# Kernel optimization log

Measured on AMD Instinct MI355X. Metric: run time of the kernel, lower is better.

## Reference

```python
import jax, jax.numpy as jnp
import numpy as np

N, E = 20000, 100000
IN_CH, HID_CH, EDGE_DIM, NUM_CLASSES = 32, 32, 16, 10


def setup_inputs() -> dict:
    key = jax.random.key(0)
    ks = jax.random.split(key, 20)
    s = 0.05
    inp = {
        "x": jax.random.normal(ks[0], (N, IN_CH), jnp.float32),
        "edge_index": jax.random.randint(ks[1], (2, E), 0, N, jnp.int64),
        "edge_attr": jax.random.normal(ks[2], (E, EDGE_DIM), jnp.float32),
        # edge MLP 1: edge_dim -> in*hid -> in*hid (weights stored as (in, out))
        "e1_w1": jax.random.normal(ks[3], (EDGE_DIM, IN_CH * HID_CH), jnp.float32) * s,
        "e1_b1": jnp.zeros((IN_CH * HID_CH,), jnp.float32),
        "e1_w2": jax.random.normal(ks[4], (IN_CH * HID_CH, IN_CH * HID_CH), jnp.float32) * s,
        "e1_b2": jnp.zeros((IN_CH * HID_CH,), jnp.float32),
        "root1": jax.random.normal(ks[5], (IN_CH, HID_CH), jnp.float32) * s,
        "bias1": jnp.zeros((HID_CH,), jnp.float32),
        # edge MLP 2: edge_dim -> hid*hid -> hid*hid
        "e2_w1": jax.random.normal(ks[6], (EDGE_DIM, HID_CH * HID_CH), jnp.float32) * s,
        "e2_b1": jnp.zeros((HID_CH * HID_CH,), jnp.float32),
        "e2_w2": jax.random.normal(ks[7], (HID_CH * HID_CH, HID_CH * HID_CH), jnp.float32) * s,
        "e2_b2": jnp.zeros((HID_CH * HID_CH,), jnp.float32),
        "root2": jax.random.normal(ks[8], (HID_CH, HID_CH), jnp.float32) * s,
        "bias2": jnp.zeros((HID_CH,), jnp.float32),
        "lin_w": jax.random.normal(ks[9], (HID_CH, NUM_CLASSES), jnp.float32) * s,
        "lin_b": jnp.zeros((NUM_CLASSES,), jnp.float32),
    }
    return inp


def _nnconv_mean(x, src, dst, edge_attr, w1, b1, w2, b2, root, bias, in_ch, out_ch, n_nodes):
    # edge MLP -> per-edge weight matrix [E, in_ch, out_ch]
    h = jax.nn.relu(edge_attr @ w1 + b1) @ w2 + b2
    W = h.reshape(-1, in_ch, out_ch)
    # message: x_j @ W_e (gather source features, per-edge matmul)
    msg = jnp.einsum('ei,eio->eo', x[src], W)
    # scatter-mean to target nodes
    agg = jax.ops.segment_sum(msg, dst, num_segments=n_nodes)
    cnt = jax.ops.segment_sum(jnp.ones((msg.shape[0],), msg.dtype), dst, num_segments=n_nodes)
    mean = agg / jnp.maximum(cnt, 1.0)[:, None]
    return mean + x @ root + bias


def reference(x, edge_index, edge_attr,
              e1_w1, e1_b1, e1_w2, e1_b2, root1, bias1,
              e2_w1, e2_b1, e2_w2, e2_b2, root2, bias2,
              lin_w, lin_b):
    src, dst = edge_index[0], edge_index[1]
    n = x.shape[0]
    h = jax.nn.relu(_nnconv_mean(x, src, dst, edge_attr, e1_w1, e1_b1, e1_w2, e1_b2,
                                 root1, bias1, IN_CH, HID_CH, n))
    # dropout p=0.5 is identity in eval mode
    h = jax.nn.relu(_nnconv_mean(h, src, dst, edge_attr, e2_w1, e2_b1, e2_w2, e2_b2,
                                 root2, bias2, HID_CH, HID_CH, n))
    return h @ lin_w + lin_b
```

## Files before the change

kernel.cpp:

```cpp
#include <hip/hip_runtime.h>

typedef __attribute__((ext_vector_type(8))) short sh8;
typedef __attribute__((ext_vector_type(4))) float f32x4;

#define E_EDGES 100000
#define E_PAD   100096
#define N_NODES 20000

__device__ __forceinline__ unsigned short f2bf(float f) {
  union { float f; unsigned int u; } v; v.f = f;
  unsigned int r = v.u + 0x7FFFu + ((v.u >> 16) & 1u);
  return (unsigned short)(r >> 16);
}

__device__ __forceinline__ void async16(const void* g, void* l) {
  __builtin_amdgcn_global_load_lds((const __attribute__((address_space(1))) unsigned int*)g,
                                   (__attribute__((address_space(3))) unsigned int*)l,
                                   16, 0, 0);
}

__global__ void transpose_w2_kernel(const float* __restrict__ w2, unsigned short* __restrict__ w2t) {
  __shared__ float tile[32][33];
  int b = blockIdx.x;
  int bx = b & 31, by = b >> 5;
  int lx = threadIdx.x & 31, ly = threadIdx.x >> 5;
#pragma unroll
  for (int j = 0; j < 4; ++j)
    tile[ly + j*8][lx] = w2[(by*32 + ly + j*8)*1024 + bx*32 + lx];
  __syncthreads();
#pragma unroll
  for (int j = 0; j < 4; ++j)
    w2t[(size_t)(bx*32 + ly + j*8)*1024 + by*32 + lx] = f2bf(tile[lx][ly + j*8]);
}

__global__ __launch_bounds__(256)
void edge_mlp1_kernel(const float* __restrict__ ea, const float* __restrict__ w1,
                      const float* __restrict__ b1, unsigned short* __restrict__ h1) {
  __shared__ float eas[8][16];
  const int tid = threadIdx.x;
  const int e0 = blockIdx.x * 8;
  if (tid < 128) {
    int g = tid >> 4, d = tid & 15;
    int ge = e0 + g;
    eas[g][d] = (ge < E_EDGES) ? ea[(size_t)ge*16 + d] : 0.f;
  }
  __syncthreads();
  const int c0 = tid * 4;
  float4 bb = *(const float4*)(b1 + c0);
  float4 acc[8];
#pragma unroll
  for (int g = 0; g < 8; ++g) acc[g] = bb;
#pragma unroll
  for (int d = 0; d < 16; ++d) {
    float4 w = *(const float4*)(w1 + (size_t)d*1024 + c0);
#pragma unroll
    for (int g = 0; g < 8; ++g) {
      float ev = eas[g][d];
      acc[g].x += ev*w.x; acc[g].y += ev*w.y; acc[g].z += ev*w.z; acc[g].w += ev*w.w;
    }
  }
#pragma unroll
  for (int g = 0; g < 8; ++g) {
    ushort4 o;
    if (e0 + g < E_EDGES) {
      o.x = f2bf(fmaxf(acc[g].x, 0.f)); o.y = f2bf(fmaxf(acc[g].y, 0.f));
      o.z = f2bf(fmaxf(acc[g].z, 0.f)); o.w = f2bf(fmaxf(acc[g].w, 0.f));
    } else {
      o.x = o.y = o.z = o.w = 0;
    }
    *(ushort4*)(h1 + (size_t)(e0 + g)*1024 + c0) = o;
  }
}

__global__ void count_kernel(const int* __restrict__ dst, float* __restrict__ cnt) {
  int t = blockIdx.x*256 + threadIdx.x;
  if (t < E_EDGES) atomicAdd(&cnt[dst[t]], 1.0f);
}

__global__ __launch_bounds__(256, 4)
void gemm_scatter_kernel(const unsigned short* __restrict__ h1,
                         const unsigned short* __restrict__ w2t,
                         const float* __restrict__ b2,
                         const float* __restrict__ xin,
                         const int* __restrict__ src,
                         const int* __restrict__ dst,
                         float* __restrict__ agg) {
  __shared__ __align__(16) unsigned char smem[32768];
  unsigned short* Als = (unsigned short*)smem;
  unsigned short* Bls = (unsigned short*)(smem + 16384);
  float* msgbuf = (float*)smem;
  __shared__ __align__(16) float xg[128][4];
  __shared__ int dsts[128];

  const int tid  = threadIdx.x;
  const int wave = tid >> 6, lane = tid & 63;
  const int wm = wave >> 1, wn = wave & 1;
  const int lr = lane >> 4, lc = lane & 15;
  const int logical = (blockIdx.x & 7) * 782 + (blockIdx.x >> 3);
  const int tile_m = logical >> 3, tile_n = logical & 7;
  const int e0 = tile_m * 128, n0 = tile_n * 128;

  if (tid < 128) {
    int ge = e0 + tid;
    float4 v = make_float4(0.f, 0.f, 0.f, 0.f);
    if (ge < E_EDGES) {
      int s = src[ge];
      v = *(const float4*)(xin + (size_t)s*32 + tile_n*4);
    }
    *(float4*)xg[tid] = v;
  } else {
    int e = tid - 128;
    int ge = e0 + e;
    dsts[e] = (ge < E_EDGES) ? dst[ge] : -1;
  }

  f32x4 acc[4][4];
#pragma unroll
  for (int i = 0; i < 4; ++i)
#pragma unroll
    for (int j = 0; j < 4; ++j) acc[i][j] = (f32x4){0.f,0.f,0.f,0.f};

  const unsigned short* Ag = h1  + (size_t)e0*1024;
  const unsigned short* Bg = w2t + (size_t)n0*1024;
  const int srow = wave*32 + (lane >> 3);
  const int scol = (lane & 7) * 8;

  for (int kt = 0; kt < 16; ++kt) {
    const int k0 = kt * 64;
    __syncthreads();
#pragma unroll
    for (int j = 0; j < 4; ++j) {
      async16(Ag + (size_t)(srow + j*8)*1024 + k0 + scol, &Als[wave*2048 + j*512]);
      async16(Bg + (size_t)(srow + j*8)*1024 + k0 + scol, &Bls[wave*2048 + j*512]);
    }
    __syncthreads();
#pragma unroll
    for (int kk = 0; kk < 2; ++kk) {
      sh8 av[4], bv[4];
#pragma unroll
      for (int mi = 0; mi < 4; ++mi)
        av[mi] = *(const sh8*)&Als[(wm*64 + mi*16 + lc)*64 + kk*32 + lr*8];
#pragma unroll
      for (int ni = 0; ni < 4; ++ni)
        bv[ni] = *(const sh8*)&Bls[(wn*64 + ni*16 + lc)*64 + kk*32 + lr*8];
#pragma unroll
      for (int mi = 0; mi < 4; ++mi)
#pragma unroll
        for (int ni = 0; ni < 4; ++ni)
          acc[mi][ni] = __builtin_amdgcn_mfma_f32_16x16x32_bf16(av[mi], bv[ni], acc[mi][ni], 0, 0, 0);
    }
  }

  float b2c[4];
#pragma unroll
  for (int ni = 0; ni < 4; ++ni) b2c[ni] = b2[n0 + wn*64 + ni*16 + lc];

  float ms0[4][4], ms1[4][4];
#pragma unroll
  for (int mi = 0; mi < 4; ++mi)
#pragma unroll
    for (int r = 0; r < 4; ++r) {
      int e = wm*64 + mi*16 + lr*4 + r;
      float x0 = xg[e][2*wn], x1 = xg[e][2*wn + 1];
      ms0[mi][r] = (acc[mi][0][r] + b2c[0])*x0 + (acc[mi][2][r] + b2c[2])*x1;
      ms1[mi][r] = (acc[mi][1][r] + b2c[1])*x0 + (acc[mi][3][r] + b2c[3])*x1;
    }

  __syncthreads();
  if (wn == 0) {
#pragma unroll
    for (int mi = 0; mi < 4; ++mi)
#pragma unroll
      for (int r = 0; r < 4; ++r) {
        int e = wm*64 + mi*16 + lr*4 + r;
        msgbuf[e*33 + lc]      = ms0[mi][r];
        msgbuf[e*33 + lc + 16] = ms1[mi][r];
      }
  }
  __syncthreads();
  if (wn == 1) {
#pragma unroll
    for (int mi = 0; mi < 4; ++mi)
#pragma unroll
      for (int r = 0; r < 4; ++r) {
        int e = wm*64 + mi*16 + lr*4 + r;
        msgbuf[e*33 + lc]      += ms0[mi][r];
        msgbuf[e*33 + lc + 16] += ms1[mi][r];
      }
  }
  __syncthreads();
  for (int t = tid; t < 128*32; t += 256) {
    int e = t >> 5, o = t & 31;
    int dn = dsts[e];
    if (dn >= 0) atomicAdd(&agg[(size_t)dn*32 + o], msgbuf[e*33 + o]);
  }
}

__global__ void node_update_kernel(const float* __restrict__ agg, const float* __restrict__ cnt,
                                   const float* __restrict__ xin, const float* __restrict__ root,
                                   const float* __restrict__ bias, float* __restrict__ outp) {
  int t = blockIdx.x*256 + threadIdx.x;
  if (t >= N_NODES*32) return;
  int n = t >> 5, i = t & 31;
  const float* xr = xin + (size_t)n*32;
  float s = bias[i];
#pragma unroll
  for (int j = 0; j < 32; ++j) s += xr[j]*root[j*32 + i];
  float c = cnt[n]; c = c > 1.f ? c : 1.f;
  float v = agg[t]/c + s;
  outp[t] = fmaxf(v, 0.f);
}

__global__ void final_linear_kernel(const float* __restrict__ h, const float* __restrict__ lw,
                                    const float* __restrict__ lb, float* __restrict__ out) {
  int t = blockIdx.x*256 + threadIdx.x;
  if (t >= N_NODES*10) return;
  int n = t / 10, k = t % 10;
  const float* hr = h + (size_t)n*32;
  float s = lb[k];
#pragma unroll
  for (int i = 0; i < 32; ++i) s += hr[i]*lw[i*10 + k];
  out[t] = s;
}

extern "C" void kernel_launch(void* const* d_in, const int* in_sizes, int n_in,
                              void* d_out, int out_size, void* d_ws, size_t ws_size,
                              hipStream_t stream) {
  const float* x     = (const float*)d_in[0];
  const int*   ei    = (const int*)d_in[1];
  const float* ea    = (const float*)d_in[2];
  const float* e1w1  = (const float*)d_in[3];
  const float* e1b1  = (const float*)d_in[4];
  const float* e1w2  = (const float*)d_in[5];
  const float* e1b2  = (const float*)d_in[6];
  const float* root1 = (const float*)d_in[7];
  const float* bias1 = (const float*)d_in[8];
  const float* e2w1  = (const float*)d_in[9];
  const float* e2b1  = (const float*)d_in[10];
  const float* e2w2  = (const float*)d_in[11];
  const float* e2b2  = (const float*)d_in[12];
  const float* root2 = (const float*)d_in[13];
  const float* bias2 = (const float*)d_in[14];
  const float* linw  = (const float*)d_in[15];
  const float* linb  = (const float*)d_in[16];
  const int* srcp = ei;
  const int* dstp = ei + E_EDGES;

  char* ws = (char*)d_ws;
  size_t off = 0;
  auto alloc = [&](size_t bytes) { void* p = ws + off; off += (bytes + 255) & ~(size_t)255; return p; };
  unsigned short* h1buf = (unsigned short*)alloc((size_t)E_PAD*1024*2);
  unsigned short* w2t   = (unsigned short*)alloc((size_t)1024*1024*2);
  float* agg  = (float*)alloc((size_t)N_NODES*32*4);
  float* cnt  = (float*)alloc((size_t)N_NODES*4);
  float* out1 = (float*)alloc((size_t)N_NODES*32*4);
  float* hbuf = (float*)alloc((size_t)N_NODES*32*4);
  (void)ws_size; (void)n_in; (void)in_sizes; (void)out_size;

  hipMemsetAsync(agg, 0, (size_t)N_NODES*32*4, stream);
  hipMemsetAsync(cnt, 0, (size_t)N_NODES*4, stream);
  count_kernel<<<(E_EDGES + 255)/256, 256, 0, stream>>>(dstp, cnt);

  transpose_w2_kernel<<<1024, 256, 0, stream>>>(e1w2, w2t);
  edge_mlp1_kernel<<<E_PAD/8, 256, 0, stream>>>(ea, e1w1, e1b1, h1buf);
  gemm_scatter_kernel<<<(E_PAD/128)*8, 256, 0, stream>>>(h1buf, w2t, e1b2, x, srcp, dstp, agg);
  node_update_kernel<<<(N_NODES*32 + 255)/256, 256, 0, stream>>>(agg, cnt, x, root1, bias1, out1);

  hipMemsetAsync(agg, 0, (size_t)N_NODES*32*4, stream);
  transpose_w2_kernel<<<1024, 256, 0, stream>>>(e2w2, w2t);
  edge_mlp1_kernel<<<E_PAD/8, 256, 0, stream>>>(ea, e2w1, e2b1, h1buf);
  gemm_scatter_kernel<<<(E_PAD/128)*8, 256, 0, stream>>>(h1buf, w2t, e2b2, out1, srcp, dstp, agg);
  node_update_kernel<<<(N_NODES*32 + 255)/256, 256, 0, stream>>>(agg, cnt, out1, root2, bias2, hbuf);

  final_linear_kernel<<<(N_NODES*10 + 255)/256, 256, 0, stream>>>(hbuf, linw, linb, (float*)d_out);
}
```

Baseline: 692.6 us.

## Double-buffer LDS, enlarge GEMM tile to 256x256, swizzle LDS in scatter GEMM

```diff
diff --git a/kernel.cpp b/kernel.cpp
--- a/kernel.cpp
+++ b/kernel.cpp
@@ -6,6 +6,10 @@
 #define E_EDGES 100000
 #define E_PAD   100096
 #define N_NODES 20000
+
+#define BAR() do { __builtin_amdgcn_sched_barrier(0); __builtin_amdgcn_s_barrier(); __builtin_amdgcn_sched_barrier(0); } while (0)
+#define WAITV0()    asm volatile("s_waitcnt vmcnt(0)" ::: "memory")
+#define WAITLGKM0() asm volatile("s_waitcnt lgkmcnt(0)" ::: "memory")
 
 __device__ __forceinline__ unsigned short f2bf(float f) {
   union { float f; unsigned int u; } v; v.f = f;
@@ -77,7 +81,7 @@
   if (t < E_EDGES) atomicAdd(&cnt[dst[t]], 1.0f);
 }
 
-__global__ __launch_bounds__(256, 4)
+__global__ __launch_bounds__(512, 2)
 void gemm_scatter_kernel(const unsigned short* __restrict__ h1,
                          const unsigned short* __restrict__ w2t,
                          const float* __restrict__ b2,
@@ -85,114 +89,125 @@
                          const int* __restrict__ src,
                          const int* __restrict__ dst,
                          float* __restrict__ agg) {
-  __shared__ __align__(16) unsigned char smem[32768];
-  unsigned short* Als = (unsigned short*)smem;
-  unsigned short* Bls = (unsigned short*)(smem + 16384);
-  float* msgbuf = (float*)smem;
-  __shared__ __align__(16) float xg[128][4];
-  __shared__ int dsts[128];
+  __shared__ __align__(16) unsigned short Als[2][256*64];
+  __shared__ __align__(16) unsigned short Bls[2][256*64];
+  float* msgA = (float*)&Als[0][0];
+  float* msgB = (float*)&Bls[0][0];
+  float (*xg)[8] = (float (*)[8])((char*)&Als[0][0] + 36864);
+  int* dsts = (int*)((char*)&Bls[0][0] + 36864);
 
   const int tid  = threadIdx.x;
   const int wave = tid >> 6, lane = tid & 63;
-  const int wm = wave >> 1, wn = wave & 1;
+  const int wm = wave >> 2, wn = wave & 3;
   const int lr = lane >> 4, lc = lane & 15;
-  const int logical = (blockIdx.x & 7) * 782 + (blockIdx.x >> 3);
-  const int tile_m = logical >> 3, tile_n = logical & 7;
-  const int e0 = tile_m * 128, n0 = tile_n * 128;
-
-  if (tid < 128) {
-    int ge = e0 + tid;
-    float4 v = make_float4(0.f, 0.f, 0.f, 0.f);
-    if (ge < E_EDGES) {
-      int s = src[ge];
-      v = *(const float4*)(xin + (size_t)s*32 + tile_n*4);
-    }
-    *(float4*)xg[tid] = v;
-  } else {
-    int e = tid - 128;
-    int ge = e0 + e;
-    dsts[e] = (ge < E_EDGES) ? dst[ge] : -1;
-  }
-
-  f32x4 acc[4][4];
-#pragma unroll
-  for (int i = 0; i < 4; ++i)
-#pragma unroll
-    for (int j = 0; j < 4; ++j) acc[i][j] = (f32x4){0.f,0.f,0.f,0.f};
+
+  const int bid = blockIdx.x;
+  const int xcd = bid & 7, idx = bid >> 3;
+  const int logical = (xcd < 4 ? xcd*196 : 784 + (xcd - 4)*195) + idx;
+  const int tile_m = logical >> 2, tile_n = logical & 3;
+  const int e0 = tile_m*256, n0 = tile_n*256;
 
   const unsigned short* Ag = h1  + (size_t)e0*1024;
   const unsigned short* Bg = w2t + (size_t)n0*1024;
-  const int srow = wave*32 + (lane >> 3);
-  const int scol = (lane & 7) * 8;
-
+
+  const int rj     = lane >> 3;
+  const int colswz = 8*((lane & 7) ^ rj);
+  const int swzb   = (lc & 7) << 4;
+
+#define STAGE(buf, kt) do {                                                         \
+    _Pragma("unroll")                                                               \
+    for (int j = 0; j < 4; ++j) {                                                   \
+      int row = (wave*4 + j)*8 + rj;                                                \
+      async16(Ag + (size_t)row*1024 + (kt)*64 + colswz, &Als[buf][(wave*4 + j)*512]); \
+      async16(Bg + (size_t)row*1024 + (kt)*64 + colswz, &Bls[buf][(wave*4 + j)*512]); \
+    }                                                                               \
+  } while (0)
+
+  f32x4 acc[8][4];
+#pragma unroll
+  for (int m = 0; m < 8; ++m)
+#pragma unroll
+    for (int n = 0; n < 4; ++n) acc[m][n] = (f32x4){0.f, 0.f, 0.f, 0.f};
+
+  STAGE(0, 0);
+
+#pragma unroll
   for (int kt = 0; kt < 16; ++kt) {
-    const int k0 = kt * 64;
-    __syncthreads();
-#pragma unroll
-    for (int j = 0; j < 4; ++j) {
-      async16(Ag + (size_t)(srow + j*8)*1024 + k0 + scol, &Als[wave*2048 + j*512]);
-      async16(Bg + (size_t)(srow + j*8)*1024 + k0 + scol, &Bls[wave*2048 + j*512]);
-    }
-    __syncthreads();
-#pragma unroll
-    for (int kk = 0; kk < 2; ++kk) {
-      sh8 av[4], bv[4];
-#pragma unroll
-      for (int mi = 0; mi < 4; ++mi)
-        av[mi] = *(const sh8*)&Als[(wm*64 + mi*16 + lc)*64 + kk*32 + lr*8];
-#pragma unroll
-      for (int ni = 0; ni < 4; ++ni)
-        bv[ni] = *(const sh8*)&Bls[(wn*64 + ni*16 + lc)*64 + kk*32 + lr*8];
-#pragma unroll
-      for (int mi = 0; mi < 4; ++mi)
-#pragma unroll
-        for (int ni = 0; ni < 4; ++ni)
-          acc[mi][ni] = __builtin_amdgcn_mfma_f32_16x16x32_bf16(av[mi], bv[ni], acc[mi][ni], 0, 0, 0);
-    }
-  }
-
+    const int cur = kt & 1;
+    WAITV0();
+    BAR();
+    const char* Ab = (const char*)&Als[cur][0];
+    const char* Bb = (const char*)&Bls[cur][0];
+    sh8 b[4][2], a[8][2];
+#pragma unroll
+    for (int n = 0; n < 4; ++n)
+#pragma unroll
+      for (int kk = 0; kk < 2; ++kk)
+        b[n][kk] = *(const sh8*)(Bb + (wn*64 + n*16 + lc)*128 + ((kk*64 + lr*16) ^ swzb));
+#pragma unroll
+    for (int m = 0; m < 8; ++m)
+#pragma unroll
+      for (int kk = 0; kk < 2; ++kk)
+        a[m][kk] = *(const sh8*)(Ab + (wm*128 + m*16 + lc)*128 + ((kk*64 + lr*16) ^ swzb));
+    WAITLGKM0();
+    BAR();
+    if (kt < 15) STAGE(cur ^ 1, kt + 1);
+    __builtin_amdgcn_s_setprio(1);
+#pragma unroll
+    for (int m = 0; m < 8; ++m)
+#pragma unroll
+      for (int n = 0; n < 4; ++n) {
+        acc[m][n] = __builtin_amdgcn_mfma_f32_16x16x32_bf16(a[m][0], b[n][0], acc[m][n], 0, 0, 0);
+        acc[m][n] = __builtin_amdgcn_mfma_f32_16x16x32_bf16(a[m][1], b[n][1], acc[m][n], 0, 0, 0);
+      }
+    __builtin_amdgcn_s_setprio(0);
+  }
+#undef STAGE
+
+  {
+    int e = tid >> 1, half = tid & 1;
+    int ge = e0 + e;
+    float4 v = make_float4(0.f, 0.f, 0.f, 0.f);
+    if (ge < E_EDGES) v = *(const float4*)(xin + (size_t)src[ge]*32 + tile_n*8 + half*4);
+    *(float4*)&xg[e][half*4] = v;
+    if (tid < 256) dsts[tid] = (e0 + tid < E_EDGES) ? dst[e0 + tid] : -1;
+  }
   float b2c[4];
 #pragma unroll
-  for (int ni = 0; ni < 4; ++ni) b2c[ni] = b2[n0 + wn*64 + ni*16 + lc];
-
-  float ms0[4][4], ms1[4][4];
-#pragma unroll
-  for (int mi = 0; mi < 4; ++mi)
-#pragma unroll
-    for (int r = 0; r < 4; ++r) {
-      int e = wm*64 + mi*16 + lr*4 + r;
-      float x0 = xg[e][2*wn], x1 = xg[e][2*wn + 1];
-      ms0[mi][r] = (acc[mi][0][r] + b2c[0])*x0 + (acc[mi][2][r] + b2c[2])*x1;
-      ms1[mi][r] = (acc[mi][1][r] + b2c[1])*x0 + (acc[mi][3][r] + b2c[3])*x1;
-    }
-
-  __syncthreads();
-  if (wn == 0) {
-#pragma unroll
-    for (int mi = 0; mi < 4; ++mi)
+  for (int n = 0; n < 4; ++n) b2c[n] = b2[n0 + wn*64 + n*16 + lc];
+  WAITLGKM0();
+  BAR();
+
+  if ((wn & 1) == 0) {
+    float* mb = (wn == 0) ? msgA : msgB;
+#pragma unroll
+    for (int m = 0; m < 8; ++m)
 #pragma unroll
       for (int r = 0; r < 4; ++r) {
-        int e = wm*64 + mi*16 + lr*4 + r;
-        msgbuf[e*33 + lc]      = ms0[mi][r];
-        msgbuf[e*33 + lc + 16] = ms1[mi][r];
+        int e = wm*128 + m*16 + lr*4 + r;
+        float x0 = xg[e][2*wn], x1 = xg[e][2*wn + 1];
+        mb[e*33 + lc]      = (acc[m][0][r] + b2c[0])*x0 + (acc[m][2][r] + b2c[2])*x1;
+        mb[e*33 + lc + 16] = (acc[m][1][r] + b2c[1])*x0 + (acc[m][3][r] + b2c[3])*x1;
       }
   }
-  __syncthreads();
-  if (wn == 1) {
-#pragma unroll
-    for (int mi = 0; mi < 4; ++mi)
+  BAR();
+  if ((wn & 1) == 1) {
+    float* mb = (wn == 1) ? msgA : msgB;
+#pragma unroll
+    for (int m = 0; m < 8; ++m)
 #pragma unroll
       for (int r = 0; r < 4; ++r) {
-        int e = wm*64 + mi*16 + lr*4 + r;
-        msgbuf[e*33 + lc]      += ms0[mi][r];
-        msgbuf[e*33 + lc + 16] += ms1[mi][r];
+        int e = wm*128 + m*16 + lr*4 + r;
+        float x0 = xg[e][2*wn], x1 = xg[e][2*wn + 1];
+        mb[e*33 + lc]      += (acc[m][0][r] + b2c[0])*x0 + (acc[m][2][r] + b2c[2])*x1;
+        mb[e*33 + lc + 16] += (acc[m][1][r] + b2c[1])*x0 + (acc[m][3][r] + b2c[3])*x1;
       }
   }
-  __syncthreads();
-  for (int t = tid; t < 128*32; t += 256) {
+  BAR();
+  for (int t = tid; t < 256*32; t += 512) {
     int e = t >> 5, o = t & 31;
     int dn = dsts[e];
-    if (dn >= 0) atomicAdd(&agg[(size_t)dn*32 + o], msgbuf[e*33 + o]);
+    if (dn >= 0) atomicAdd(&agg[(size_t)dn*32 + o], msgA[e*33 + o] + msgB[e*33 + o]);
   }
 }
 
@@ -261,15 +276,17 @@
   hipMemsetAsync(cnt, 0, (size_t)N_NODES*4, stream);
   count_kernel<<<(E_EDGES + 255)/256, 256, 0, stream>>>(dstp, cnt);
 
+  const int gemm_grid = (E_PAD/256) * 4;
+
   transpose_w2_kernel<<<1024, 256, 0, stream>>>(e1w2, w2t);
   edge_mlp1_kernel<<<E_PAD/8, 256, 0, stream>>>(ea, e1w1, e1b1, h1buf);
-  gemm_scatter_kernel<<<(E_PAD/128)*8, 256, 0, stream>>>(h1buf, w2t, e1b2, x, srcp, dstp, agg);
+  gemm_scatter_kernel<<<gemm_grid, 512, 0, stream>>>(h1buf, w2t, e1b2, x, srcp, dstp, agg);
   node_update_kernel<<<(N_NODES*32 + 255)/256, 256, 0, stream>>>(agg, cnt, x, root1, bias1, out1);
 
   hipMemsetAsync(agg, 0, (size_t)N_NODES*32*4, stream);
   transpose_w2_kernel<<<1024, 256, 0, stream>>>(e2w2, w2t);
   edge_mlp1_kernel<<<E_PAD/8, 256, 0, stream>>>(ea, e2w1, e2b1, h1buf);
-  gemm_scatter_kernel<<<(E_PAD/128)*8, 256, 0, stream>>>(h1buf, w2t, e2b2, out1, srcp, dstp, agg);
+  gemm_scatter_kernel<<<gemm_grid, 512, 0, stream>>>(h1buf, w2t, e2b2, out1, srcp, dstp, agg);
   node_update_kernel<<<(N_NODES*32 + 255)/256, 256, 0, stream>>>(agg, cnt, out1, root2, bias2, hbuf);
 
   final_linear_kernel<<<(N_NODES*10 + 255)/256, 256, 0, stream>>>(hbuf, linw, linb, (float*)d_out);
```

Result: slower. 780.1 us (+12.6%).
